# Kernel tuning notes

Measured on AMD Instinct MI355X. Metric: run time of the kernel, lower is better.

The kernel has to match this reference:

```python
import jax, jax.numpy as jnp
import numpy as np

N = 50000      # num_nodes
E = 1000000    # graph edges
EP = 400000    # pos/neg link-pred edges
H = 128        # hidden_dim
C = 768        # chemical_dim
L = 2          # num GCN layers


def setup_inputs() -> dict:
    key = jax.random.key(0)
    ks = jax.random.split(key, 12)
    edge_index = jax.random.randint(ks[0], (2, E), 0, N)
    chemistry = jax.random.normal(ks[1], (N, C), jnp.float32)
    pos_edge = jax.random.randint(ks[2], (EP, 2), 0, N)
    neg_edge = jax.random.randint(ks[3], (EP, 2), 0, N)
    smiles_mask = jax.random.uniform(ks[4], (N,), jnp.float32)
    node_emb = jax.random.normal(ks[5], (N, H), jnp.float32) * 0.1
    conv_w = jax.random.normal(ks[6], (L, H, H), jnp.float32) / np.sqrt(H)
    conv_b = jnp.zeros((L, H), jnp.float32)
    chem_w = jax.random.normal(ks[7], (C, H), jnp.float32) / np.sqrt(C)
    chem_b = jnp.zeros((H,), jnp.float32)
    dec_w1 = jax.random.normal(ks[8], (2 * H, H), jnp.float32) / np.sqrt(2 * H)
    dec_b1 = jnp.zeros((H,), jnp.float32)
    dec_w2 = jax.random.normal(ks[9], (H, 1), jnp.float32) / np.sqrt(H)
    dec_b2 = jnp.zeros((1,), jnp.float32)
    return dict(edge_index=edge_index, chemistry=chemistry, pos_edge=pos_edge,
                neg_edge=neg_edge, smiles_mask=smiles_mask, node_emb=node_emb,
                conv_w=conv_w, conv_b=conv_b, chem_w=chem_w, chem_b=chem_b,
                dec_w1=dec_w1, dec_b1=dec_b1, dec_w2=dec_w2, dec_b2=dec_b2)


def reference(edge_index, chemistry, pos_edge, neg_edge, smiles_mask, node_emb,
              conv_w, conv_b, chem_w, chem_b, dec_w1, dec_b1, dec_w2, dec_b2):
    row, col = edge_index[0], edge_index[1]  # src -> dst
    # GCN symmetric normalization (add_self_loops=False)
    deg = jax.ops.segment_sum(jnp.ones((E,), jnp.float32), col, num_segments=N)
    dinv = jnp.where(deg > 0, 1.0 / jnp.sqrt(jnp.maximum(deg, 1.0)), 0.0)
    norm = dinv[row] * dinv[col]  # [E]

    # Encoder: structure-only GCN over learned node embeddings
    z = node_emb
    for l in range(L):
        h = z @ conv_w[l]                       # [N,H]
        msg = h[row] * norm[:, None]            # gather [E,H]
        agg = jax.ops.segment_sum(msg, col, num_segments=N)  # scatter-add
        z = jax.nn.relu(agg + conv_b[l])

    # Chemistry projection, masked by smiles validity
    c = jax.nn.relu(chemistry @ chem_w + chem_b) * smiles_mask[:, None]  # [N,H]

    def decode(edges):
        src, dst = edges[:, 0], edges[:, 1]
        f = jnp.concatenate([z[src] * z[dst], c[src] * c[dst]], axis=-1)  # [Ep,2H]
        hmid = jax.nn.relu(f @ dec_w1 + dec_b1)
        return (hmid @ dec_w2 + dec_b2)[:, 0]

    return decode(pos_edge), decode(neg_edge)
```

## Files before the change

### kernel.cpp

```cpp
#include <hip/hip_runtime.h>
#include <hip/hip_bf16.h>

#define NN 50000
#define NE 1000000
#define NEP 400000
#define HD 128
#define CD 768
#define NB_SCAN 196
#define FSTR 256

typedef __attribute__((ext_vector_type(8))) short bf16x8;
typedef __attribute__((ext_vector_type(4))) float f32x4;

__device__ __forceinline__ ushort f2bf(float x) {
    unsigned u = __float_as_uint(x);
    u += 0x7FFF + ((u >> 16) & 1);
    return (ushort)(u >> 16);
}
__device__ __forceinline__ float bf2f(ushort b) {
    return __uint_as_float(((unsigned)b) << 16);
}
__device__ __forceinline__ unsigned pk2bf(float a, float b) {
    __hip_bfloat162 h = __float22bfloat162_rn(make_float2(a, b));
    return *(unsigned*)&h;
}
__device__ __forceinline__ bf16x8 pack8(float4 a0, float4 a1) {
    union { unsigned u[4]; bf16x8 v; } r;
    r.u[0] = pk2bf(a0.x, a0.y);
    r.u[1] = pk2bf(a0.z, a0.w);
    r.u[2] = pk2bf(a1.x, a1.y);
    r.u[3] = pk2bf(a1.z, a1.w);
    return r.v;
}

__global__ __launch_bounds__(256) void count_kernel(const int* __restrict__ col,
                                                    int* __restrict__ cnt) {
    int i = blockIdx.x * 256 + threadIdx.x;
    if (i < NE) atomicAdd(&cnt[col[i]], 1);
}

__global__ __launch_bounds__(256) void dinv_kernel(const int* __restrict__ cnt,
                                                   float* __restrict__ dinv) {
    int i = blockIdx.x * 256 + threadIdx.x;
    if (i < NN) {
        int d = cnt[i];
        dinv[i] = (d > 0) ? 1.0f / sqrtf((float)d) : 0.0f;
    }
}

__global__ __launch_bounds__(256) void scan1_kernel(const int* __restrict__ cnt,
                                                    int* __restrict__ partial,
                                                    int* __restrict__ bsum) {
    __shared__ int s[256];
    int i = blockIdx.x * 256 + threadIdx.x;
    int v = (i < NN) ? cnt[i] : 0;
    s[threadIdx.x] = v;
    __syncthreads();
    for (int o = 1; o < 256; o <<= 1) {
        int t = (threadIdx.x >= o) ? s[threadIdx.x - o] : 0;
        __syncthreads();
        s[threadIdx.x] += t;
        __syncthreads();
    }
    if (i < NN) partial[i] = s[threadIdx.x] - v;
    if (threadIdx.x == 255) bsum[blockIdx.x] = s[255];
}

__global__ __launch_bounds__(256) void scan2_kernel(int* __restrict__ bsum) {
    __shared__ int s[256];
    int v = (threadIdx.x < NB_SCAN) ? bsum[threadIdx.x] : 0;
    s[threadIdx.x] = v;
    __syncthreads();
    for (int o = 1; o < 256; o <<= 1) {
        int t = (threadIdx.x >= o) ? s[threadIdx.x - o] : 0;
        __syncthreads();
        s[threadIdx.x] += t;
        __syncthreads();
    }
    if (threadIdx.x < NB_SCAN) bsum[threadIdx.x] = s[threadIdx.x] - v;
}

__global__ __launch_bounds__(256) void scan3_kernel(const int* __restrict__ partial,
                                                    const int* __restrict__ bsum,
                                                    int* __restrict__ off,
                                                    int* __restrict__ cursor) {
    int i = blockIdx.x * 256 + threadIdx.x;
    if (i < NN) {
        int o = partial[i] + bsum[blockIdx.x];
        off[i] = o;
        cursor[i] = o;
    }
}

__global__ __launch_bounds__(256) void fill_kernel(const int* __restrict__ row,
                                                   const int* __restrict__ col,
                                                   const float* __restrict__ dinv,
                                                   int* __restrict__ cursor,
                                                   int* __restrict__ csr_idx,
                                                   float* __restrict__ csr_w) {
    int e = blockIdx.x * 256 + threadIdx.x;
    if (e < NE) {
        int c = col[e], r = row[e];
        int slot = atomicAdd(&cursor[c], 1);
        csr_idx[slot] = r;
        csr_w[slot] = dinv[r];
    }
}

__global__ __launch_bounds__(256) void wfrag_kernel(const float* __restrict__ w,
                                                    ushort* __restrict__ wf) {
    int tid = blockIdx.x * 256 + threadIdx.x;
    int ks = tid >> 9, nt = (tid >> 6) & 7, l = tid & 63;
    int kbase = ks * 32 + ((l >> 4) << 3);
    int colq = nt * 16 + (l & 15);
    ushort r[8];
#pragma unroll
    for (int j = 0; j < 8; ++j) r[j] = f2bf(w[(size_t)(kbase + j) * HD + colq]);
    *(uint4*)&wf[(size_t)tid * 8] = *(uint4*)r;
}

template <int KS, bool EPI>
__global__ __launch_bounds__(256) void feat_mfma_kernel(const float* __restrict__ A,
                                                        const ushort* __restrict__ wf,
                                                        const float* __restrict__ bias,
                                                        const float* __restrict__ mask,
                                                        ushort* __restrict__ out,
                                                        int ostride, int ooff) {
    __shared__ float At[64][36];
    const int t = threadIdx.x;
    const int w = t >> 6, lane = t & 63;
    const int rowBase = blockIdx.x * 64;
    const int nt0 = w * 2;
    const int K = KS * 32;

    f32x4 acc[4][2] = {};

    for (int ks = 0; ks < KS; ++ks) {
        __syncthreads();
#pragma unroll
        for (int i = 0; i < 2; ++i) {
            int li = t + i * 256;
            int r = li >> 3, c4 = li & 7;
            int grow = rowBase + r;
            float4 v = make_float4(0.f, 0.f, 0.f, 0.f);
            if (grow < NN) v = *(const float4*)&A[(size_t)grow * K + ks * 32 + c4 * 4];
            *(float4*)&At[r][c4 * 4] = v;
        }
        __syncthreads();
        bf16x8 bf0 = ((const bf16x8*)wf)[(ks * 8 + nt0) * 64 + lane];
        bf16x8 bf1 = ((const bf16x8*)wf)[(ks * 8 + nt0 + 1) * 64 + lane];
#pragma unroll
        for (int mt = 0; mt < 4; ++mt) {
            int row = mt * 16 + (lane & 15);
            float4 a0 = *(const float4*)&At[row][(lane >> 4) * 8];
            float4 a1 = *(const float4*)&At[row][(lane >> 4) * 8 + 4];
            bf16x8 af = pack8(a0, a1);
            acc[mt][0] = __builtin_amdgcn_mfma_f32_16x16x32_bf16(af, bf0, acc[mt][0], 0, 0, 0);
            acc[mt][1] = __builtin_amdgcn_mfma_f32_16x16x32_bf16(af, bf1, acc[mt][1], 0, 0, 0);
        }
    }

    const int c0 = lane & 15, rq = lane >> 4;
    float bb0 = EPI ? bias[nt0 * 16 + c0] : 0.f;
    float bb1 = EPI ? bias[nt0 * 16 + 16 + c0] : 0.f;
#pragma unroll
    for (int mt = 0; mt < 4; ++mt) {
#pragma unroll
        for (int reg = 0; reg < 4; ++reg) {
            int grow = rowBase + mt * 16 + rq * 4 + reg;
            if (grow < NN) {
                float v0 = acc[mt][0][reg], v1 = acc[mt][1][reg];
                if (EPI) {
                    float m = mask[grow];
                    v0 = fmaxf(v0 + bb0, 0.f) * m;
                    v1 = fmaxf(v1 + bb1, 0.f) * m;
                }
                out[(size_t)grow * ostride + ooff + nt0 * 16 + c0] = f2bf(v0);
                out[(size_t)grow * ostride + ooff + nt0 * 16 + 16 + c0] = f2bf(v1);
            }
        }
    }
}

template <bool BF16OUT>
__global__ __launch_bounds__(256) void gather_kernel(const int* __restrict__ off,
                                                     const int* __restrict__ cnt,
                                                     const int* __restrict__ csr_idx,
                                                     const float* __restrict__ csr_w,
                                                     const float* __restrict__ dinv,
                                                     const ushort* __restrict__ h,
                                                     const float* __restrict__ bias,
                                                     float* __restrict__ z,
                                                     ushort* __restrict__ zb,
                                                     int ostride) {
    int v = blockIdx.x * 4 + (threadIdx.x >> 6);
    if (v >= NN) return;
    int lane = threadIdx.x & 63;
    int s = off[v];
    int e = s + cnt[v];
    float accx = 0.f, accy = 0.f;
    for (; s + 3 < e; s += 4) {
        int r0 = csr_idx[s], r1 = csr_idx[s + 1], r2 = csr_idx[s + 2], r3 = csr_idx[s + 3];
        float w0 = csr_w[s], w1 = csr_w[s + 1], w2 = csr_w[s + 2], w3 = csr_w[s + 3];
        unsigned u0 = *(const unsigned*)&h[(size_t)r0 * HD + lane * 2];
        unsigned u1 = *(const unsigned*)&h[(size_t)r1 * HD + lane * 2];
        unsigned u2 = *(const unsigned*)&h[(size_t)r2 * HD + lane * 2];
        unsigned u3 = *(const unsigned*)&h[(size_t)r3 * HD + lane * 2];
        accx = fmaf(bf2f((ushort)u0), w0, accx); accy = fmaf(bf2f((ushort)(u0 >> 16)), w0, accy);
        accx = fmaf(bf2f((ushort)u1), w1, accx); accy = fmaf(bf2f((ushort)(u1 >> 16)), w1, accy);
        accx = fmaf(bf2f((ushort)u2), w2, accx); accy = fmaf(bf2f((ushort)(u2 >> 16)), w2, accy);
        accx = fmaf(bf2f((ushort)u3), w3, accx); accy = fmaf(bf2f((ushort)(u3 >> 16)), w3, accy);
    }
    for (; s < e; ++s) {
        int r0 = csr_idx[s];
        float w0 = csr_w[s];
        unsigned u0 = *(const unsigned*)&h[(size_t)r0 * HD + lane * 2];
        accx = fmaf(bf2f((ushort)u0), w0, accx); accy = fmaf(bf2f((ushort)(u0 >> 16)), w0, accy);
    }
    float dv = dinv[v];
    float2 b = *(const float2*)&bias[lane * 2];
    float ox = fmaxf(fmaf(accx, dv, b.x), 0.f);
    float oy = fmaxf(fmaf(accy, dv, b.y), 0.f);
    if (BF16OUT) {
        *(unsigned*)&zb[(size_t)v * ostride + lane * 2] = pk2bf(ox, oy);
    } else {
        float2 o; o.x = ox; o.y = oy;
        *(float2*)&z[(size_t)v * HD + lane * 2] = o;
    }
}

__global__ __launch_bounds__(256) void decode_mfma_kernel(const int* __restrict__ pos_edge,
                                                          const int* __restrict__ neg_edge,
                                                          const ushort* __restrict__ feat,
                                                          const ushort* __restrict__ w1f,
                                                          const float* __restrict__ b1,
                                                          const float* __restrict__ w2,
                                                          const float* __restrict__ b2,
                                                          float* __restrict__ out) {
    __shared__ ushort Flds[8 * 4 * 64 * 8];
    __shared__ int sEdge[128];
    __shared__ float part[4][64];
    const int t = threadIdx.x;
    const int w = t >> 6, lane = t & 63;
    const int bid = blockIdx.x;
    const bool isPos = bid < (NEP / 64);
    const int* edges = isPos ? pos_edge : neg_edge;
    const int ebase = (isPos ? bid : bid - NEP / 64) * 64;
    float* op = out + (isPos ? 0 : NEP);

    if (t < 128) sEdge[t] = edges[(size_t)ebase * 2 + t];
    __syncthreads();

    const int seg = t & 31, eslot = t >> 5;
#pragma unroll
    for (int it = 0; it < 8; ++it) {
        int e = it * 8 + eslot;
        int s = sEdge[2 * e], dd = sEdge[2 * e + 1];
        uint4 av = *(const uint4*)&feat[(size_t)s * FSTR + seg * 8];
        uint4 bv = *(const uint4*)&feat[(size_t)dd * FSTR + seg * 8];
        const ushort* ap = (const ushort*)&av;
        const ushort* bp = (const ushort*)&bv;
        uint4 res;
        res.x = pk2bf(bf2f(ap[0]) * bf2f(bp[0]), bf2f(ap[1]) * bf2f(bp[1]));
        res.y = pk2bf(bf2f(ap[2]) * bf2f(bp[2]), bf2f(ap[3]) * bf2f(bp[3]));
        res.z = pk2bf(bf2f(ap[4]) * bf2f(bp[4]), bf2f(ap[5]) * bf2f(bp[5]));
        res.w = pk2bf(bf2f(ap[6]) * bf2f(bp[6]), bf2f(ap[7]) * bf2f(bp[7]));
        int ks = seg >> 2;
        int mt = e >> 4;
        int fl = (e & 15) | ((seg & 3) << 4);
        int swz = (seg & 3) | ((ks & 1) << 2);
        ((uint4*)Flds)[(ks * 4 + mt) * 64 + (fl ^ swz)] = res;
    }
    __syncthreads();

    f32x4 acc[4][2] = {};
    const int nt0 = w * 2;
#pragma unroll
    for (int ks = 0; ks < 8; ++ks) {
        bf16x8 bf0 = ((const bf16x8*)w1f)[(ks * 8 + nt0) * 64 + lane];
        bf16x8 bf1 = ((const bf16x8*)w1f)[(ks * 8 + nt0 + 1) * 64 + lane];
        const int rswz = ((lane >> 4) & 3) | ((ks & 1) << 2);
#pragma unroll
        for (int mt = 0; mt < 4; ++mt) {
            bf16x8 af = ((const bf16x8*)Flds)[(ks * 4 + mt) * 64 + (lane ^ rswz)];
            acc[mt][0] = __builtin_amdgcn_mfma_f32_16x16x32_bf16(af, bf0, acc[mt][0], 0, 0, 0);
            acc[mt][1] = __builtin_amdgcn_mfma_f32_16x16x32_bf16(af, bf1, acc[mt][1], 0, 0, 0);
        }
    }

    const int c0 = lane & 15, rq = lane >> 4;
    float b1v0 = b1[nt0 * 16 + c0], b1v1 = b1[nt0 * 16 + 16 + c0];
    float w2v0 = w2[nt0 * 16 + c0], w2v1 = w2[nt0 * 16 + 16 + c0];
#pragma unroll
    for (int mt = 0; mt < 4; ++mt) {
#pragma unroll
        for (int reg = 0; reg < 4; ++reg) {
            float h0 = fmaxf(acc[mt][0][reg] + b1v0, 0.f);
            float h1 = fmaxf(acc[mt][1][reg] + b1v1, 0.f);
            float p = fmaf(h0, w2v0, h1 * w2v1);
            p += __shfl_xor(p, 1);
            p += __shfl_xor(p, 2);
            p += __shfl_xor(p, 4);
            p += __shfl_xor(p, 8);
            if (c0 == 0) part[w][mt * 16 + rq * 4 + reg] = p;
        }
    }
    __syncthreads();
    if (t < 64) {
        op[ebase + t] = part[0][t] + part[1][t] + part[2][t] + part[3][t] + b2[0];
    }
}

extern "C" void kernel_launch(void* const* d_in, const int* in_sizes, int n_in,
                              void* d_out, int out_size, void* d_ws, size_t ws_size,
                              hipStream_t stream) {
    const int* edge_index = (const int*)d_in[0];
    const float* chemistry = (const float*)d_in[1];
    const int* pos_edge = (const int*)d_in[2];
    const int* neg_edge = (const int*)d_in[3];
    const float* smiles_mask = (const float*)d_in[4];
    const float* node_emb = (const float*)d_in[5];
    const float* conv_w = (const float*)d_in[6];
    const float* conv_b = (const float*)d_in[7];
    const float* chem_w = (const float*)d_in[8];
    const float* chem_b = (const float*)d_in[9];
    const float* dec_w1 = (const float*)d_in[10];
    const float* dec_b1 = (const float*)d_in[11];
    const float* dec_w2 = (const float*)d_in[12];
    const float* dec_b2 = (const float*)d_in[13];
    float* out = (float*)d_out;

    char* ws = (char*)d_ws;
    int* cnt = (int*)(ws + 0);
    float* dinv = (float*)(ws + 204800);
    int* partial = (int*)(ws + 409600);
    int* off = (int*)(ws + 614400);
    int* cursor = (int*)(ws + 819200);
    int* bsum = (int*)(ws + 1024000);
    int* csr_idx = (int*)(ws + 1048576);
    float* csr_w = (float*)(ws + 5242880);
    float* bufZ = (float*)(ws + 9437184);
    ushort* hb = (ushort*)(ws + 35037184);
    ushort* feat = (ushort*)(ws + 47837184);
    ushort* w1f = (ushort*)(ws + 73437184);
    ushort* wcf = (ushort*)(ws + 73502720);
    ushort* wc0f = (ushort*)(ws + 73699328);
    ushort* wc1f = (ushort*)(ws + 73732096);

    const int* e_row = edge_index;
    const int* e_col = edge_index + NE;

    hipMemsetAsync(cnt, 0, (size_t)NN * 4, stream);
    count_kernel<<<(NE + 255) / 256, 256, 0, stream>>>(e_col, cnt);
    dinv_kernel<<<(NN + 255) / 256, 256, 0, stream>>>(cnt, dinv);
    scan1_kernel<<<NB_SCAN, 256, 0, stream>>>(cnt, partial, bsum);
    scan2_kernel<<<1, 256, 0, stream>>>(bsum);
    scan3_kernel<<<NB_SCAN, 256, 0, stream>>>(partial, bsum, off, cursor);
    fill_kernel<<<(NE + 255) / 256, 256, 0, stream>>>(e_row, e_col, dinv, cursor, csr_idx, csr_w);
    wfrag_kernel<<<16, 256, 0, stream>>>(dec_w1, w1f);
    wfrag_kernel<<<48, 256, 0, stream>>>(chem_w, wcf);
    wfrag_kernel<<<8, 256, 0, stream>>>(conv_w, wc0f);
    wfrag_kernel<<<8, 256, 0, stream>>>(conv_w + HD * HD, wc1f);

    const int mmGrid = (NN + 63) / 64;
    const int gaGrid = (NN + 3) / 4;

    feat_mfma_kernel<4, false><<<mmGrid, 256, 0, stream>>>(node_emb, wc0f, nullptr, nullptr, hb, HD, 0);
    gather_kernel<false><<<gaGrid, 256, 0, stream>>>(off, cnt, csr_idx, csr_w, dinv, hb, conv_b, bufZ, nullptr, 0);

    feat_mfma_kernel<4, false><<<mmGrid, 256, 0, stream>>>(bufZ, wc1f, nullptr, nullptr, hb, HD, 0);
    gather_kernel<true><<<gaGrid, 256, 0, stream>>>(off, cnt, csr_idx, csr_w, dinv, hb, conv_b + HD, nullptr, feat, FSTR);

    feat_mfma_kernel<24, true><<<mmGrid, 256, 0, stream>>>(chemistry, wcf, chem_b, smiles_mask, feat, FSTR, HD);

    decode_mfma_kernel<<<2 * (NEP / 64), 256, 0, stream>>>(pos_edge, neg_edge, feat, w1f,
                                                           dec_b1, dec_w2, dec_b2, out);
}
```

Before: 460.5 us.

## Switch intermediate storage and MFMA from bf16 to fp16 with packed multiplies

Replaces bf16 with fp16 for the stored features, weights and MFMA operands. The decoder elementwise products now use packed half multiplies instead of unpacking to float and repacking, and all feature loads are batched ahead of the compute loop to raise memory-level parallelism. Launch bounds with a minimum-occupancy hint are added to the decoder. The cost is fp16's smaller range with round-toward-zero conversion, which could overflow or lose accuracy, and the register pressure from holding 16 uint4 loads at once.

```diff
diff --git a/kernel.cpp b/kernel.cpp
--- a/kernel.cpp
+++ b/kernel.cpp
@@ -1,5 +1,5 @@
 #include <hip/hip_runtime.h>
-#include <hip/hip_bf16.h>
+#include <hip/hip_fp16.h>
 
 #define NN 50000
 #define NE 1000000
@@ -9,28 +9,35 @@
 #define NB_SCAN 196
 #define FSTR 256
 
-typedef __attribute__((ext_vector_type(8))) short bf16x8;
+typedef _Float16 f16x8 __attribute__((ext_vector_type(8)));
+typedef _Float16 f16x2 __attribute__((ext_vector_type(2)));
+typedef __fp16 hf16x2 __attribute__((ext_vector_type(2)));
 typedef __attribute__((ext_vector_type(4))) float f32x4;
 
-__device__ __forceinline__ ushort f2bf(float x) {
-    unsigned u = __float_as_uint(x);
-    u += 0x7FFF + ((u >> 16) & 1);
-    return (ushort)(u >> 16);
-}
-__device__ __forceinline__ float bf2f(ushort b) {
-    return __uint_as_float(((unsigned)b) << 16);
-}
-__device__ __forceinline__ unsigned pk2bf(float a, float b) {
-    __hip_bfloat162 h = __float22bfloat162_rn(make_float2(a, b));
-    return *(unsigned*)&h;
-}
-__device__ __forceinline__ bf16x8 pack8(float4 a0, float4 a1) {
-    union { unsigned u[4]; bf16x8 v; } r;
-    r.u[0] = pk2bf(a0.x, a0.y);
-    r.u[1] = pk2bf(a0.z, a0.w);
-    r.u[2] = pk2bf(a1.x, a1.y);
-    r.u[3] = pk2bf(a1.z, a1.w);
+__device__ __forceinline__ unsigned pk2h(float a, float b) {
+    hf16x2 p = __builtin_amdgcn_cvt_pkrtz(a, b);
+    return __builtin_bit_cast(unsigned, p);
+}
+__device__ __forceinline__ ushort f2h(float x) {
+    return (ushort)(pk2h(x, 0.f) & 0xffffu);
+}
+__device__ __forceinline__ unsigned h2mul(unsigned a, unsigned b) {
+    f16x2 ha = __builtin_bit_cast(f16x2, a);
+    f16x2 hb = __builtin_bit_cast(f16x2, b);
+    f16x2 r = ha * hb;
+    return __builtin_bit_cast(unsigned, r);
+}
+__device__ __forceinline__ f16x8 pack8h(float4 a0, float4 a1) {
+    union { unsigned u[4]; f16x8 v; } r;
+    r.u[0] = pk2h(a0.x, a0.y);
+    r.u[1] = pk2h(a0.z, a0.w);
+    r.u[2] = pk2h(a1.x, a1.y);
+    r.u[3] = pk2h(a1.z, a1.w);
     return r.v;
+}
+__device__ __forceinline__ float2 h2f2(unsigned u) {
+    f16x2 h = __builtin_bit_cast(f16x2, u);
+    return make_float2((float)h[0], (float)h[1]);
 }
 
 __global__ __launch_bounds__(256) void count_kernel(const int* __restrict__ col,
@@ -115,7 +122,7 @@
     int colq = nt * 16 + (l & 15);
     ushort r[8];
 #pragma unroll
-    for (int j = 0; j < 8; ++j) r[j] = f2bf(w[(size_t)(kbase + j) * HD + colq]);
+    for (int j = 0; j < 8; ++j) r[j] = f2h(w[(size_t)(kbase + j) * HD + colq]);
     *(uint4*)&wf[(size_t)tid * 8] = *(uint4*)r;
 }
 
@@ -147,16 +154,16 @@
             *(float4*)&At[r][c4 * 4] = v;
         }
         __syncthreads();
-        bf16x8 bf0 = ((const bf16x8*)wf)[(ks * 8 + nt0) * 64 + lane];
-        bf16x8 bf1 = ((const bf16x8*)wf)[(ks * 8 + nt0 + 1) * 64 + lane];
+        f16x8 bf0 = ((const f16x8*)wf)[(ks * 8 + nt0) * 64 + lane];
+        f16x8 bf1 = ((const f16x8*)wf)[(ks * 8 + nt0 + 1) * 64 + lane];
 #pragma unroll
         for (int mt = 0; mt < 4; ++mt) {
             int row = mt * 16 + (lane & 15);
             float4 a0 = *(const float4*)&At[row][(lane >> 4) * 8];
             float4 a1 = *(const float4*)&At[row][(lane >> 4) * 8 + 4];
-            bf16x8 af = pack8(a0, a1);
-            acc[mt][0] = __builtin_amdgcn_mfma_f32_16x16x32_bf16(af, bf0, acc[mt][0], 0, 0, 0);
-            acc[mt][1] = __builtin_amdgcn_mfma_f32_16x16x32_bf16(af, bf1, acc[mt][1], 0, 0, 0);
+            f16x8 af = pack8h(a0, a1);
+            acc[mt][0] = __builtin_amdgcn_mfma_f32_16x16x32_f16(af, bf0, acc[mt][0], 0, 0, 0);
+            acc[mt][1] = __builtin_amdgcn_mfma_f32_16x16x32_f16(af, bf1, acc[mt][1], 0, 0, 0);
         }
     }
 
@@ -175,14 +182,14 @@
                     v0 = fmaxf(v0 + bb0, 0.f) * m;
                     v1 = fmaxf(v1 + bb1, 0.f) * m;
                 }
-                out[(size_t)grow * ostride + ooff + nt0 * 16 + c0] = f2bf(v0);
-                out[(size_t)grow * ostride + ooff + nt0 * 16 + 16 + c0] = f2bf(v1);
+                out[(size_t)grow * ostride + ooff + nt0 * 16 + c0] = f2h(v0);
+                out[(size_t)grow * ostride + ooff + nt0 * 16 + 16 + c0] = f2h(v1);
             }
         }
     }
 }
 
-template <bool BF16OUT>
+template <bool F16OUT>
 __global__ __launch_bounds__(256) void gather_kernel(const int* __restrict__ off,
                                                      const int* __restrict__ cnt,
                                                      const int* __restrict__ csr_idx,
@@ -206,37 +213,38 @@
         unsigned u1 = *(const unsigned*)&h[(size_t)r1 * HD + lane * 2];
         unsigned u2 = *(const unsigned*)&h[(size_t)r2 * HD + lane * 2];
         unsigned u3 = *(const unsigned*)&h[(size_t)r3 * HD + lane * 2];
-        accx = fmaf(bf2f((ushort)u0), w0, accx); accy = fmaf(bf2f((ushort)(u0 >> 16)), w0, accy);
-        accx = fmaf(bf2f((ushort)u1), w1, accx); accy = fmaf(bf2f((ushort)(u1 >> 16)), w1, accy);
-        accx = fmaf(bf2f((ushort)u2), w2, accx); accy = fmaf(bf2f((ushort)(u2 >> 16)), w2, accy);
-        accx = fmaf(bf2f((ushort)u3), w3, accx); accy = fmaf(bf2f((ushort)(u3 >> 16)), w3, accy);
+        float2 f0 = h2f2(u0), f1 = h2f2(u1), f2 = h2f2(u2), f3 = h2f2(u3);
+        accx = fmaf(f0.x, w0, accx); accy = fmaf(f0.y, w0, accy);
+        accx = fmaf(f1.x, w1, accx); accy = fmaf(f1.y, w1, accy);
+        accx = fmaf(f2.x, w2, accx); accy = fmaf(f2.y, w2, accy);
+        accx = fmaf(f3.x, w3, accx); accy = fmaf(f3.y, w3, accy);
     }
     for (; s < e; ++s) {
         int r0 = csr_idx[s];
         float w0 = csr_w[s];
-        unsigned u0 = *(const unsigned*)&h[(size_t)r0 * HD + lane * 2];
-        accx = fmaf(bf2f((ushort)u0), w0, accx); accy = fmaf(bf2f((ushort)(u0 >> 16)), w0, accy);
+        float2 f0 = h2f2(*(const unsigned*)&h[(size_t)r0 * HD + lane * 2]);
+        accx = fmaf(f0.x, w0, accx); accy = fmaf(f0.y, w0, accy);
     }
     float dv = dinv[v];
     float2 b = *(const float2*)&bias[lane * 2];
     float ox = fmaxf(fmaf(accx, dv, b.x), 0.f);
     float oy = fmaxf(fmaf(accy, dv, b.y), 0.f);
-    if (BF16OUT) {
-        *(unsigned*)&zb[(size_t)v * ostride + lane * 2] = pk2bf(ox, oy);
+    if (F16OUT) {
+        *(unsigned*)&zb[(size_t)v * ostride + lane * 2] = pk2h(ox, oy);
     } else {
         float2 o; o.x = ox; o.y = oy;
         *(float2*)&z[(size_t)v * HD + lane * 2] = o;
     }
 }
 
-__global__ __launch_bounds__(256) void decode_mfma_kernel(const int* __restrict__ pos_edge,
-                                                          const int* __restrict__ neg_edge,
-                                                          const ushort* __restrict__ feat,
-                                                          const ushort* __restrict__ w1f,
-                                                          const float* __restrict__ b1,
-                                                          const float* __restrict__ w2,
-                                                          const float* __restrict__ b2,
-                                                          float* __restrict__ out) {
+__global__ __launch_bounds__(256, 4) void decode_mfma_kernel(const int* __restrict__ pos_edge,
+                                                             const int* __restrict__ neg_edge,
+                                                             const ushort* __restrict__ feat,
+                                                             const ushort* __restrict__ w1f,
+                                                             const float* __restrict__ b1,
+                                                             const float* __restrict__ w2,
+                                                             const float* __restrict__ b2,
+                                                             float* __restrict__ out) {
     __shared__ ushort Flds[8 * 4 * 64 * 8];
     __shared__ int sEdge[128];
     __shared__ float part[4][64];
@@ -252,19 +260,22 @@
     __syncthreads();
 
     const int seg = t & 31, eslot = t >> 5;
+    uint4 avr[8], bvr[8];
 #pragma unroll
     for (int it = 0; it < 8; ++it) {
         int e = it * 8 + eslot;
         int s = sEdge[2 * e], dd = sEdge[2 * e + 1];
-        uint4 av = *(const uint4*)&feat[(size_t)s * FSTR + seg * 8];
-        uint4 bv = *(const uint4*)&feat[(size_t)dd * FSTR + seg * 8];
-        const ushort* ap = (const ushort*)&av;
-        const ushort* bp = (const ushort*)&bv;
+        avr[it] = *(const uint4*)&feat[(size_t)s * FSTR + seg * 8];
+        bvr[it] = *(const uint4*)&feat[(size_t)dd * FSTR + seg * 8];
+    }
+#pragma unroll
+    for (int it = 0; it < 8; ++it) {
+        int e = it * 8 + eslot;
         uint4 res;
-        res.x = pk2bf(bf2f(ap[0]) * bf2f(bp[0]), bf2f(ap[1]) * bf2f(bp[1]));
-        res.y = pk2bf(bf2f(ap[2]) * bf2f(bp[2]), bf2f(ap[3]) * bf2f(bp[3]));
-        res.z = pk2bf(bf2f(ap[4]) * bf2f(bp[4]), bf2f(ap[5]) * bf2f(bp[5]));
-        res.w = pk2bf(bf2f(ap[6]) * bf2f(bp[6]), bf2f(ap[7]) * bf2f(bp[7]));
+        res.x = h2mul(avr[it].x, bvr[it].x);
+        res.y = h2mul(avr[it].y, bvr[it].y);
+        res.z = h2mul(avr[it].z, bvr[it].z);
+        res.w = h2mul(avr[it].w, bvr[it].w);
         int ks = seg >> 2;
         int mt = e >> 4;
         int fl = (e & 15) | ((seg & 3) << 4);
@@ -277,14 +288,14 @@
     const int nt0 = w * 2;
 #pragma unroll
     for (int ks = 0; ks < 8; ++ks) {
-        bf16x8 bf0 = ((const bf16x8*)w1f)[(ks * 8 + nt0) * 64 + lane];
-        bf16x8 bf1 = ((const bf16x8*)w1f)[(ks * 8 + nt0 + 1) * 64 + lane];
+        f16x8 bf0 = ((const f16x8*)w1f)[(ks * 8 + nt0) * 64 + lane];
+        f16x8 bf1 = ((const f16x8*)w1f)[(ks * 8 + nt0 + 1) * 64 + lane];
         const int rswz = ((lane >> 4) & 3) | ((ks & 1) << 2);
 #pragma unroll
         for (int mt = 0; mt < 4; ++mt) {
-            bf16x8 af = ((const bf16x8*)Flds)[(ks * 4 + mt) * 64 + (lane ^ rswz)];
-            acc[mt][0] = __builtin_amdgcn_mfma_f32_16x16x32_bf16(af, bf0, acc[mt][0], 0, 0, 0);
-            acc[mt][1] = __builtin_amdgcn_mfma_f32_16x16x32_bf16(af, bf1, acc[mt][1], 0, 0, 0);
+            f16x8 af = ((const f16x8*)Flds)[(ks * 4 + mt) * 64 + (lane ^ rswz)];
+            acc[mt][0] = __builtin_amdgcn_mfma_f32_16x16x32_f16(af, bf0, acc[mt][0], 0, 0, 0);
+            acc[mt][1] = __builtin_amdgcn_mfma_f32_16x16x32_f16(af, bf1, acc[mt][1], 0, 0, 0);
         }
     }
 
```

Measured after the change: 451.8 us. Within noise of the previous version (-1.9%).
